# Performance work log

Hardware: AMD Instinct MI355X
Metric: run time of the kernel (lower is better)

## Reference

```python
import jax, jax.numpy as jnp
import numpy as np

D = 64          # feature dim
H_POS = 64      # pos_mlp hidden
H_ATTN = 4 * D  # attn_mlp hidden
B, N = 1, 1024


def setup_inputs() -> dict:
    key = jax.random.key(0)
    ks = jax.random.split(key, 12)
    s = lambda fan_in: 1.0 / np.sqrt(fan_in)
    return {
        "x": jax.random.normal(ks[0], (B, N, D), jnp.float32),
        "pos": jax.random.normal(ks[1], (B, N, 2), jnp.float32),
        "Wq": jax.random.normal(ks[2], (D, D), jnp.float32) * s(D),
        "Wk": jax.random.normal(ks[3], (D, D), jnp.float32) * s(D),
        "Wv": jax.random.normal(ks[4], (D, D), jnp.float32) * s(D),
        "pW1": jax.random.normal(ks[5], (2, H_POS), jnp.float32) * s(2),
        "pb1": jnp.zeros((H_POS,), jnp.float32),
        "pW2": jax.random.normal(ks[6], (H_POS, D), jnp.float32) * s(H_POS),
        "pb2": jnp.zeros((D,), jnp.float32),
        "aW1": jax.random.normal(ks[7], (D, H_ATTN), jnp.float32) * s(D),
        "ab1": jnp.zeros((H_ATTN,), jnp.float32),
        "aW2": jax.random.normal(ks[8], (H_ATTN, D), jnp.float32) * s(H_ATTN),
        "ab2": jnp.zeros((D,), jnp.float32),
    }


def reference(x, pos, Wq, Wk, Wv, pW1, pb1, pW2, pb2, aW1, ab1, aW2, ab2):
    # projections: [b, n, d]
    q = x @ Wq
    k = x @ Wk
    v = x @ Wv
    # pairwise relative positions: [b, i, j, 2]
    rel_pos = pos[:, :, None, :] - pos[:, None, :, :]
    # pos MLP: [b, i, j, d]
    rpe = jax.nn.relu(rel_pos @ pW1 + pb1) @ pW2 + pb2
    # pairwise q - k: [b, i, j, d]
    qk_rel = q[:, :, None, :] - k[:, None, :, :]
    # values broadcast over i, plus positional embedding: [b, i, j, d]
    vv = v[:, None, :, :] + rpe
    # attention MLP on (qk_rel + rpe): [b, i, j, d]
    sim = jax.nn.relu((qk_rel + rpe) @ aW1 + ab1) @ aW2 + ab2
    # softmax over j (axis=-2), per-channel
    attn = jax.nn.softmax(sim, axis=-2)
    # weighted aggregation: [b, i, d]
    agg = jnp.einsum('bijd,bijd->bid', attn, vv)
    return agg
```

## Files before the change

### kernel.cpp

```cpp
#include <hip/hip_runtime.h>


typedef float f32x4 __attribute__((ext_vector_type(4)));
using sh8 = __attribute__((ext_vector_type(8))) short;

static constexpr int NPTS = 1024;

static constexpr size_t BEXT_OFF = 0;
static constexpr size_t AW2F_OFF = 65536;
static constexpr size_t PW2F_OFF = 98304;
static constexpr size_t CARR_OFF = 106496;
static constexpr size_t AI_OFF   = 107520;
static constexpr size_t QI_OFF   = 369664;
static constexpr size_t VPT_OFF  = 631808;
static constexpr size_t AJ_OFF   = 893952;
static constexpr size_t KN_OFF   = 1025024;

__device__ __forceinline__ unsigned short f2b_rne(float f) {
    unsigned u = __float_as_uint(f);
    u += 0x7fffu + ((u >> 16) & 1u);
    return (unsigned short)(u >> 16);
}
__device__ __forceinline__ unsigned pk2(float lo, float hi) {
    return __builtin_amdgcn_perm(__float_as_uint(hi), __float_as_uint(lo), 0x07060302);
}
__device__ __forceinline__ float b2f(unsigned short s) {
    return __uint_as_float(((unsigned)s) << 16);
}

__global__ void prep_all(const float* __restrict__ x, const float* __restrict__ pos,
                         const float* __restrict__ Wq, const float* __restrict__ Wk,
                         const float* __restrict__ Wv, const float* __restrict__ pW1,
                         const float* __restrict__ pb1, const float* __restrict__ pW2,
                         const float* __restrict__ pb2, const float* __restrict__ aW1,
                         const float* __restrict__ ab1, const float* __restrict__ aW2,
                         unsigned short* __restrict__ bextf, unsigned short* __restrict__ aw2f,
                         unsigned short* __restrict__ pw2f, float* __restrict__ cArr,
                         float* __restrict__ qI, unsigned short* __restrict__ kN,
                         float* __restrict__ vPT, float* __restrict__ aI,
                         unsigned short* __restrict__ aJ)
{
    const int b = blockIdx.x;
    if (b < 209) {
        const int idx = b * 256 + threadIdx.x;
        if (idx < 32768) {
            const int k = idx >> 8, t = idx & 255;
            float val;
            if (k < 64) {
                float s = 0.f;
                for (int d = 0; d < 64; ++d) s = fmaf(pW2[k * 64 + d], aW1[d * 256 + t], s);
                val = s;
            } else {
                val = aW1[(k - 64) * 256 + t];
            }
            const int kc = k >> 5, kl = k & 31, qq = kl >> 3, e = kl & 7;
            const int ntg = t >> 4, tl = t & 15;
            bextf[(((size_t)(kc * 16 + ntg) * 64) + (qq * 16 + tl)) * 8 + e] = f2b_rne(val);
        } else if (idx < 49152) {
            const int r = idx - 32768;
            const int kp = r >> 6, d = r & 63;
            const int t = 64 * (kp >> 6) + 16 * (kp & 3) + ((kp >> 2) & 15);
            const int kc = kp >> 5, kl = kp & 31, qq = kl >> 3, e = kl & 7;
            const int nt = d >> 4, dl = d & 15;
            aw2f[(((size_t)(kc * 4 + nt) * 64) + (qq * 16 + dl)) * 8 + e] = f2b_rne(aW2[t * 64 + d]);
        } else if (idx < 53248) {
            const int r = idx - 49152;
            const int k = r >> 6, d = r & 63;
            const int kc = k >> 5, kl = k & 31, qq = kl >> 3, e = kl & 7;
            const int nt = d >> 4, dl = d & 15;
            pw2f[(((size_t)(kc * 4 + nt) * 64) + (qq * 16 + dl)) * 8 + e] = f2b_rne(pW2[k * 64 + d]);
        } else if (idx < 53504) {
            const int t = idx - 53248;
            float s = ab1[t];
            for (int d = 0; d < 64; ++d) s = fmaf(pb2[d], aW1[d * 256 + t], s);
            cArr[t] = s;
        }
    } else {
        const int t = threadIdx.x, sub = t >> 6, d = t & 63;
        const int i = (b - 209) * 4 + sub;
        __shared__ float xs[4][64];
        xs[sub][d] = x[i * 64 + d];
        __syncthreads();
        float q = 0.f, k = 0.f, v = 0.f;
        for (int e = 0; e < 64; ++e) {
            const float xe = xs[sub][e];
            q = fmaf(xe, Wq[e * 64 + d], q);
            k = fmaf(xe, Wk[e * 64 + d], k);
            v = fmaf(xe, Wv[e * 64 + d], v);
        }
        const float a = pos[i * 2] * pW1[d] + pos[i * 2 + 1] * pW1[64 + d];
        qI[i * 64 + d] = q;
        kN[i * 64 + d] = f2b_rne(-k);
        vPT[d * NPTS + i] = v + pb2[d];
        aI[i * 64 + d] = a + pb1[d];
        aJ[i * 64 + d] = f2b_rne(a);
    }
}

__global__ __launch_bounds__(256, 2) void ptl_main(
    const float* __restrict__ aI, const float* __restrict__ qI,
    const unsigned short* __restrict__ aJ, const unsigned short* __restrict__ kN,
    const float* __restrict__ vPT,
    const unsigned short* __restrict__ bextf, const unsigned short* __restrict__ aw2f,
    const unsigned short* __restrict__ pw2f, const float* __restrict__ cArr,
    float* __restrict__ out)
{
    const int i    = blockIdx.x;
    const int tid  = threadIdx.x;
    const int w    = tid >> 6;
    const int lane = tid & 63;
    const int m    = lane & 15;
    const int q    = lane >> 4;

    __shared__ __align__(16) uint4 AfL[2][2][4][64];
    __shared__ __align__(16) unsigned char Hs[2][2][16 * 528];

    sh8 Bf[16];
#pragma unroll
    for (int kc = 0; kc < 4; ++kc)
#pragma unroll
        for (int nt = 0; nt < 4; ++nt)
            Bf[kc * 4 + nt] = *(const sh8*)(bextf + ((size_t)((kc * 16 + 4 * w + nt) * 64 + lane)) * 8);
    sh8 W2f[8];
#pragma unroll
    for (int kc = 0; kc < 8; ++kc)
        W2f[kc] = *(const sh8*)(aw2f + ((size_t)((kc * 4 + w) * 64 + lane)) * 8);
    sh8 P2f[2];
#pragma unroll
    for (int kc = 0; kc < 2; ++kc)
        P2f[kc] = *(const sh8*)(pw2f + ((size_t)((kc * 4 + w) * 64 + lane)) * 8);

    f32x4 cvec[4];
#pragma unroll
    for (int nt = 0; nt < 4; ++nt) {
        const float c = cArr[64 * w + 16 * nt + m];
        cvec[nt] = (f32x4){c, c, c, c};
    }

    const int  half   = w & 1;
    const bool isRelu = (w < 2);
    const unsigned short* bsrc  = (isRelu ? aJ : kN) + m * 64 + half * 32 + q * 8;
    const float*          ibase = (isRelu ? aI : qI) + i * 64 + half * 32 + q * 8;
    float iv[8];
    *(float4*)(iv)     = *(const float4*)(ibase);
    *(float4*)(iv + 4) = *(const float4*)(ibase + 4);

#pragma unroll
    for (int s = 0; s < 2; ++s) {
        const sh8 raw = *(const sh8*)(bsrc + (size_t)(16 * s) * 64);
        float t[8];
#pragma unroll
        for (int e = 0; e < 8; ++e)
            t[e] = isRelu ? fmaxf(iv[e] - b2f((unsigned short)raw[e]), 0.f)
                          : iv[e] + b2f((unsigned short)raw[e]);
        uint4 pk;
        pk.x = pk2(t[0], t[1]); pk.y = pk2(t[2], t[3]);
        pk.z = pk2(t[4], t[5]); pk.w = pk2(t[6], t[7]);
        AfL[0][s][w][lane] = pk;
    }
    __syncthreads();

    float num = 0.f, den = 0.f;
    const f32x4 z4 = {0.f, 0.f, 0.f, 0.f};
    const float* vbase = vPT + (size_t)(16 * w + m) * NPTS;

    for (int n = 0; n < 32; ++n) {
        const int pb = n & 1, nb = pb ^ 1;
        const int j0 = n << 5;

        sh8 raw0, raw1;
        if (n < 31) {
            raw0 = *(const sh8*)(bsrc + (size_t)(j0 + 32) * 64);
            raw1 = *(const sh8*)(bsrc + (size_t)(j0 + 48) * 64);
        }
        const float4 vj0 = *(const float4*)(vbase + j0 + 4 * q);
        const float4 vj1 = *(const float4*)(vbase + j0 + 16 + 4 * q);

        const sh8 A00 = *(const sh8*)&AfL[pb][0][0][lane];
        const sh8 A01 = *(const sh8*)&AfL[pb][0][1][lane];
        const sh8 A02 = *(const sh8*)&AfL[pb][0][2][lane];
        const sh8 A03 = *(const sh8*)&AfL[pb][0][3][lane];
        {
            f32x4 acc[4];
#pragma unroll
            for (int nt = 0; nt < 4; ++nt) {
                acc[nt] = __builtin_amdgcn_mfma_f32_16x16x32_bf16(A00, Bf[0 * 4 + nt], cvec[nt], 0, 0, 0);
                acc[nt] = __builtin_amdgcn_mfma_f32_16x16x32_bf16(A01, Bf[1 * 4 + nt], acc[nt], 0, 0, 0);
                acc[nt] = __builtin_amdgcn_mfma_f32_16x16x32_bf16(A02, Bf[2 * 4 + nt], acc[nt], 0, 0, 0);
                acc[nt] = __builtin_amdgcn_mfma_f32_16x16x32_bf16(A03, Bf[3 * 4 + nt], acc[nt], 0, 0, 0);
            }
            unsigned char* hw = Hs[pb][0] + (4 * q) * 528 + 128 * w + 8 * m;
#pragma unroll
            for (int r = 0; r < 4; ++r) {
                uint2 pk;
                pk.x = pk2(fmaxf(acc[0][r], 0.f), fmaxf(acc[1][r], 0.f));
                pk.y = pk2(fmaxf(acc[2][r], 0.f), fmaxf(acc[3][r], 0.f));
                *(uint2*)(hw + r * 528) = pk;
            }
        }

        const sh8 A10 = *(const sh8*)&AfL[pb][1][0][lane];
        const sh8 A11 = *(const sh8*)&AfL[pb][1][1][lane];
        const sh8 A12 = *(const sh8*)&AfL[pb][1][2][lane];
        const sh8 A13 = *(const sh8*)&AfL[pb][1][3][lane];
        {
            f32x4 acc[4];
#pragma unroll
            for (int nt = 0; nt < 4; ++nt) {
                acc[nt] = __builtin_amdgcn_mfma_f32_16x16x32_bf16(A10, Bf[0 * 4 + nt], cvec[nt], 0, 0, 0);
                acc[nt] = __builtin_amdgcn_mfma_f32_16x16x32_bf16(A11, Bf[1 * 4 + nt], acc[nt], 0, 0, 0);
                acc[nt] = __builtin_amdgcn_mfma_f32_16x16x32_bf16(A12, Bf[2 * 4 + nt], acc[nt], 0, 0, 0);
                acc[nt] = __builtin_amdgcn_mfma_f32_16x16x32_bf16(A13, Bf[3 * 4 + nt], acc[nt], 0, 0, 0);
            }
            unsigned char* hw = Hs[pb][1] + (4 * q) * 528 + 128 * w + 8 * m;
#pragma unroll
            for (int r = 0; r < 4; ++r) {
                uint2 pk;
                pk.x = pk2(fmaxf(acc[0][r], 0.f), fmaxf(acc[1][r], 0.f));
                pk.y = pk2(fmaxf(acc[2][r], 0.f), fmaxf(acc[3][r], 0.f));
                *(uint2*)(hw + r * 528) = pk;
            }
        }

        if (n < 31) {
#pragma unroll
            for (int s = 0; s < 2; ++s) {
                const sh8 raw = s ? raw1 : raw0;
                float t[8];
#pragma unroll
                for (int e = 0; e < 8; ++e)
                    t[e] = isRelu ? fmaxf(iv[e] - b2f((unsigned short)raw[e]), 0.f)
                                  : iv[e] + b2f((unsigned short)raw[e]);
                uint4 pk;
                pk.x = pk2(t[0], t[1]); pk.y = pk2(t[2], t[3]);
                pk.z = pk2(t[4], t[5]); pk.w = pk2(t[6], t[7]);
                AfL[nb][s][w][lane] = pk;
            }
        }

        __syncthreads();

        {
            f32x4 accS = z4;
#pragma unroll
            for (int kc = 0; kc < 8; ++kc) {
                const sh8 hf = *(const sh8*)(Hs[pb][0] + m * 528 + kc * 64 + 16 * q);
                accS = __builtin_amdgcn_mfma_f32_16x16x32_bf16(hf, W2f[kc], accS, 0, 0, 0);
            }
            const f32x4 vc = {vj0.x, vj0.y, vj0.z, vj0.w};
            f32x4 accR = __builtin_amdgcn_mfma_f32_16x16x32_bf16(A00, P2f[0], vc, 0, 0, 0);
            accR = __builtin_amdgcn_mfma_f32_16x16x32_bf16(A01, P2f[1], accR, 0, 0, 0);
#pragma unroll
            for (int r = 0; r < 4; ++r) {
                const float ex = __expf(accS[r]);
                num = fmaf(ex, accR[r], num);
                den += ex;
            }
        }
        {
            f32x4 accS = z4;
#pragma unroll
            for (int kc = 0; kc < 8; ++kc) {
                const sh8 hf = *(const sh8*)(Hs[pb][1] + m * 528 + kc * 64 + 16 * q);
                accS = __builtin_amdgcn_mfma_f32_16x16x32_bf16(hf, W2f[kc], accS, 0, 0, 0);
            }
            const f32x4 vc = {vj1.x, vj1.y, vj1.z, vj1.w};
            f32x4 accR = __builtin_amdgcn_mfma_f32_16x16x32_bf16(A10, P2f[0], vc, 0, 0, 0);
            accR = __builtin_amdgcn_mfma_f32_16x16x32_bf16(A11, P2f[1], accR, 0, 0, 0);
#pragma unroll
            for (int r = 0; r < 4; ++r) {
                const float ex = __expf(accS[r]);
                num = fmaf(ex, accR[r], num);
                den += ex;
            }
        }
    }

    num += __shfl_xor(num, 16);
    num += __shfl_xor(num, 32);
    den += __shfl_xor(den, 16);
    den += __shfl_xor(den, 32);
    if (q == 0) out[i * 64 + 16 * w + m] = num / den;
}

extern "C" void kernel_launch(void* const* d_in, const int* in_sizes, int n_in,
                              void* d_out, int out_size, void* d_ws, size_t ws_size,
                              hipStream_t stream) {
    const float* x   = (const float*)d_in[0];
    const float* pos = (const float*)d_in[1];
    const float* Wq  = (const float*)d_in[2];
    const float* Wk  = (const float*)d_in[3];
    const float* Wv  = (const float*)d_in[4];
    const float* pW1 = (const float*)d_in[5];
    const float* pb1 = (const float*)d_in[6];
    const float* pW2 = (const float*)d_in[7];
    const float* pb2 = (const float*)d_in[8];
    const float* aW1 = (const float*)d_in[9];
    const float* ab1 = (const float*)d_in[10];
    const float* aW2 = (const float*)d_in[11];

    char* ws = (char*)d_ws;
    unsigned short* bextf = (unsigned short*)(ws + BEXT_OFF);
    unsigned short* aw2f  = (unsigned short*)(ws + AW2F_OFF);
    unsigned short* pw2f  = (unsigned short*)(ws + PW2F_OFF);
    float*          cArr  = (float*)(ws + CARR_OFF);
    float*          aIa   = (float*)(ws + AI_OFF);
    float*          qIa   = (float*)(ws + QI_OFF);
    float*          vPTa  = (float*)(ws + VPT_OFF);
    unsigned short* aJa   = (unsigned short*)(ws + AJ_OFF);
    unsigned short* kNa   = (unsigned short*)(ws + KN_OFF);

    prep_all<<<465, 256, 0, stream>>>(x, pos, Wq, Wk, Wv, pW1, pb1, pW2, pb2, aW1, ab1, aW2,
                                      bextf, aw2f, pw2f, cArr, qIa, kNa, vPTa, aIa, aJa);
    ptl_main<<<NPTS, 256, 0, stream>>>(aIa, qIa, aJa, kNa, vPTa, bextf, aw2f, pw2f, cArr,
                                       (float*)d_out);
}
```

Baseline: 193.0 us.

## Precompute q·aW1 and k·aW1 projections to halve first-layer MFMA K dimension

```diff
diff --git a/kernel.cpp b/kernel.cpp
--- a/kernel.cpp
+++ b/kernel.cpp
@@ -7,14 +7,13 @@
 static constexpr int NPTS = 1024;
 
 static constexpr size_t BEXT_OFF = 0;
-static constexpr size_t AW2F_OFF = 65536;
-static constexpr size_t PW2F_OFF = 98304;
-static constexpr size_t CARR_OFF = 106496;
-static constexpr size_t AI_OFF   = 107520;
-static constexpr size_t QI_OFF   = 369664;
-static constexpr size_t VPT_OFF  = 631808;
-static constexpr size_t AJ_OFF   = 893952;
-static constexpr size_t KN_OFF   = 1025024;
+static constexpr size_t AW2F_OFF = 32768;
+static constexpr size_t PW2F_OFF = 65536;
+static constexpr size_t AI_OFF   = 73728;
+static constexpr size_t AJ_OFF   = 335872;
+static constexpr size_t VPT_OFF  = 466944;
+static constexpr size_t CQ_OFF   = 729088;
+static constexpr size_t KAT_OFF  = 1777664;
 
 __device__ __forceinline__ unsigned short f2b_rne(float f) {
     unsigned u = __float_as_uint(f);
@@ -35,51 +34,41 @@
                          const float* __restrict__ pb2, const float* __restrict__ aW1,
                          const float* __restrict__ ab1, const float* __restrict__ aW2,
                          unsigned short* __restrict__ bextf, unsigned short* __restrict__ aw2f,
-                         unsigned short* __restrict__ pw2f, float* __restrict__ cArr,
-                         float* __restrict__ qI, unsigned short* __restrict__ kN,
-                         float* __restrict__ vPT, float* __restrict__ aI,
-                         unsigned short* __restrict__ aJ)
+                         unsigned short* __restrict__ pw2f,
+                         float* __restrict__ aI, unsigned short* __restrict__ aJ,
+                         float* __restrict__ vPT, float* __restrict__ cq,
+                         float* __restrict__ kaT)
 {
     const int b = blockIdx.x;
-    if (b < 209) {
+    if (b < 144) {
         const int idx = b * 256 + threadIdx.x;
-        if (idx < 32768) {
+        if (idx < 16384) {
             const int k = idx >> 8, t = idx & 255;
-            float val;
-            if (k < 64) {
-                float s = 0.f;
-                for (int d = 0; d < 64; ++d) s = fmaf(pW2[k * 64 + d], aW1[d * 256 + t], s);
-                val = s;
-            } else {
-                val = aW1[(k - 64) * 256 + t];
-            }
+            float s = 0.f;
+            for (int d = 0; d < 64; ++d) s = fmaf(pW2[k * 64 + d], aW1[d * 256 + t], s);
             const int kc = k >> 5, kl = k & 31, qq = kl >> 3, e = kl & 7;
             const int ntg = t >> 4, tl = t & 15;
-            bextf[(((size_t)(kc * 16 + ntg) * 64) + (qq * 16 + tl)) * 8 + e] = f2b_rne(val);
-        } else if (idx < 49152) {
-            const int r = idx - 32768;
+            bextf[(((size_t)(kc * 16 + ntg) * 64) + (qq * 16 + tl)) * 8 + e] = f2b_rne(s);
+        } else if (idx < 32768) {
+            const int r = idx - 16384;
             const int kp = r >> 6, d = r & 63;
             const int t = 64 * (kp >> 6) + 16 * (kp & 3) + ((kp >> 2) & 15);
             const int kc = kp >> 5, kl = kp & 31, qq = kl >> 3, e = kl & 7;
             const int nt = d >> 4, dl = d & 15;
-            aw2f[(((size_t)(kc * 4 + nt) * 64) + (qq * 16 + dl)) * 8 + e] = f2b_rne(aW2[t * 64 + d]);
-        } else if (idx < 53248) {
-            const int r = idx - 49152;
+            aw2f[(((size_t)(kc * 4 + nt) * 64) + (qq * 16 + dl)) * 8 + e] =
+                f2b_rne(aW2[t * 64 + d] * 1.4426950408889634f);
+        } else if (idx < 36864) {
+            const int r = idx - 32768;
             const int k = r >> 6, d = r & 63;
             const int kc = k >> 5, kl = k & 31, qq = kl >> 3, e = kl & 7;
             const int nt = d >> 4, dl = d & 15;
             pw2f[(((size_t)(kc * 4 + nt) * 64) + (qq * 16 + dl)) * 8 + e] = f2b_rne(pW2[k * 64 + d]);
-        } else if (idx < 53504) {
-            const int t = idx - 53248;
-            float s = ab1[t];
-            for (int d = 0; d < 64; ++d) s = fmaf(pb2[d], aW1[d * 256 + t], s);
-            cArr[t] = s;
         }
     } else {
-        const int t = threadIdx.x, sub = t >> 6, d = t & 63;
-        const int i = (b - 209) * 4 + sub;
-        __shared__ float xs[4][64];
-        xs[sub][d] = x[i * 64 + d];
+        const int tid = threadIdx.x, sub = tid >> 6, d = tid & 63;
+        const int i0 = (b - 144) * 4;
+        __shared__ float xs[4][64], qs[4][64], ks[4][64];
+        xs[sub][d] = x[(i0 + sub) * 64 + d];
         __syncthreads();
         float q = 0.f, k = 0.f, v = 0.f;
         for (int e = 0; e < 64; ++e) {
@@ -88,22 +77,45 @@
             k = fmaf(xe, Wk[e * 64 + d], k);
             v = fmaf(xe, Wv[e * 64 + d], v);
         }
-        const float a = pos[i * 2] * pW1[d] + pos[i * 2 + 1] * pW1[64 + d];
-        qI[i * 64 + d] = q;
-        kN[i * 64 + d] = f2b_rne(-k);
-        vPT[d * NPTS + i] = v + pb2[d];
-        aI[i * 64 + d] = a + pb1[d];
-        aJ[i * 64 + d] = f2b_rne(a);
+        const float a = pos[(i0 + sub) * 2] * pW1[d] + pos[(i0 + sub) * 2 + 1] * pW1[64 + d];
+        qs[sub][d] = q;
+        ks[sub][d] = k;
+        vPT[d * NPTS + i0 + sub] = v + pb2[d];
+        aI[(i0 + sub) * 64 + d] = a + pb1[d];
+        aJ[(i0 + sub) * 64 + d] = f2b_rne(a);
+        __syncthreads();
+        const int t = tid;
+        float c = ab1[t];
+        float qa0 = 0.f, qa1 = 0.f, qa2 = 0.f, qa3 = 0.f;
+        float ka0 = 0.f, ka1 = 0.f, ka2 = 0.f, ka3 = 0.f;
+        for (int dd = 0; dd < 64; ++dd) {
+            const float wv = aW1[dd * 256 + t];
+            c   = fmaf(pb2[dd],   wv, c);
+            qa0 = fmaf(qs[0][dd], wv, qa0);
+            qa1 = fmaf(qs[1][dd], wv, qa1);
+            qa2 = fmaf(qs[2][dd], wv, qa2);
+            qa3 = fmaf(qs[3][dd], wv, qa3);
+            ka0 = fmaf(ks[0][dd], wv, ka0);
+            ka1 = fmaf(ks[1][dd], wv, ka1);
+            ka2 = fmaf(ks[2][dd], wv, ka2);
+            ka3 = fmaf(ks[3][dd], wv, ka3);
+        }
+        cq[(i0 + 0) * 256 + t] = c + qa0;
+        cq[(i0 + 1) * 256 + t] = c + qa1;
+        cq[(i0 + 2) * 256 + t] = c + qa2;
+        cq[(i0 + 3) * 256 + t] = c + qa3;
+        float4 kn;
+        kn.x = -ka0; kn.y = -ka1; kn.z = -ka2; kn.w = -ka3;
+        *(float4*)(kaT + (size_t)t * NPTS + i0) = kn;
     }
 }
 
 __global__ __launch_bounds__(256, 2) void ptl_main(
-    const float* __restrict__ aI, const float* __restrict__ qI,
-    const unsigned short* __restrict__ aJ, const unsigned short* __restrict__ kN,
-    const float* __restrict__ vPT,
+    const float* __restrict__ aI, const unsigned short* __restrict__ aJ,
+    const float* __restrict__ vPT, const float* __restrict__ cq,
+    const float* __restrict__ kaT,
     const unsigned short* __restrict__ bextf, const unsigned short* __restrict__ aw2f,
-    const unsigned short* __restrict__ pw2f, const float* __restrict__ cArr,
-    float* __restrict__ out)
+    const unsigned short* __restrict__ pw2f, float* __restrict__ out)
 {
     const int i    = blockIdx.x;
     const int tid  = threadIdx.x;
@@ -111,176 +123,174 @@
     const int lane = tid & 63;
     const int m    = lane & 15;
     const int q    = lane >> 4;
-
-    __shared__ __align__(16) uint4 AfL[2][2][4][64];
+    const int js   = w >> 1;
+    const int wh   = w & 1;
+
+    __shared__ __align__(16) uint4 AfL[2][2][2][64];
     __shared__ __align__(16) unsigned char Hs[2][2][16 * 528];
-
-    sh8 Bf[16];
-#pragma unroll
-    for (int kc = 0; kc < 4; ++kc)
+    __shared__ float redN[4][2][16], redD[4][2][16];
+
+    sh8 Bf[8];
+#pragma unroll
+    for (int kc = 0; kc < 2; ++kc)
 #pragma unroll
         for (int nt = 0; nt < 4; ++nt)
             Bf[kc * 4 + nt] = *(const sh8*)(bextf + ((size_t)((kc * 16 + 4 * w + nt) * 64 + lane)) * 8);
-    sh8 W2f[8];
+    sh8 W2f[16];
 #pragma unroll
     for (int kc = 0; kc < 8; ++kc)
-        W2f[kc] = *(const sh8*)(aw2f + ((size_t)((kc * 4 + w) * 64 + lane)) * 8);
-    sh8 P2f[2];
+#pragma unroll
+        for (int nt = 0; nt < 2; ++nt)
+            W2f[kc * 2 + nt] = *(const sh8*)(aw2f + ((size_t)((kc * 4 + 2 * wh + nt) * 64 + lane)) * 8);
+    sh8 P2f[4];
 #pragma unroll
     for (int kc = 0; kc < 2; ++kc)
-        P2f[kc] = *(const sh8*)(pw2f + ((size_t)((kc * 4 + w) * 64 + lane)) * 8);
+#pragma unroll
+        for (int nt = 0; nt < 2; ++nt)
+            P2f[kc * 2 + nt] = *(const sh8*)(pw2f + ((size_t)((kc * 4 + 2 * wh + nt) * 64 + lane)) * 8);
 
     f32x4 cvec[4];
 #pragma unroll
     for (int nt = 0; nt < 4; ++nt) {
-        const float c = cArr[64 * w + 16 * nt + m];
+        const float c = cq[i * 256 + 64 * w + 16 * nt + m];
         cvec[nt] = (f32x4){c, c, c, c};
     }
 
-    const int  half   = w & 1;
-    const bool isRelu = (w < 2);
-    const unsigned short* bsrc  = (isRelu ? aJ : kN) + m * 64 + half * 32 + q * 8;
-    const float*          ibase = (isRelu ? aI : qI) + i * 64 + half * 32 + q * 8;
+    const unsigned short* bsrc  = aJ + ((size_t)(16 * js + m)) * 64 + wh * 32 + q * 8;
+    const float*          ibase = aI + i * 64 + wh * 32 + q * 8;
     float iv[8];
     *(float4*)(iv)     = *(const float4*)(ibase);
     *(float4*)(iv + 4) = *(const float4*)(ibase + 4);
 
-#pragma unroll
-    for (int s = 0; s < 2; ++s) {
-        const sh8 raw = *(const sh8*)(bsrc + (size_t)(16 * s) * 64);
+    {
+        const sh8 raw = *(const sh8*)(bsrc);
         float t[8];
 #pragma unroll
-        for (int e = 0; e < 8; ++e)
-            t[e] = isRelu ? fmaxf(iv[e] - b2f((unsigned short)raw[e]), 0.f)
-                          : iv[e] + b2f((unsigned short)raw[e]);
+        for (int e = 0; e < 8; ++e) t[e] = fmaxf(iv[e] - b2f((unsigned short)raw[e]), 0.f);
         uint4 pk;
         pk.x = pk2(t[0], t[1]); pk.y = pk2(t[2], t[3]);
         pk.z = pk2(t[4], t[5]); pk.w = pk2(t[6], t[7]);
-        AfL[0][s][w][lane] = pk;
+        AfL[0][js][wh][lane] = pk;
     }
     __syncthreads();
 
-    float num = 0.f, den = 0.f;
+    float num0 = 0.f, num1 = 0.f, den0 = 0.f, den1 = 0.f;
     const f32x4 z4 = {0.f, 0.f, 0.f, 0.f};
-    const float* vbase = vPT + (size_t)(16 * w + m) * NPTS;
+    const float* vb0 = vPT + (size_t)(32 * wh + m) * NPTS + 16 * js + 4 * q;
+    const float* vb1 = vPT + (size_t)(32 * wh + 16 + m) * NPTS + 16 * js + 4 * q;
+    const float* kbase = kaT + (size_t)(64 * w + m) * NPTS + 4 * q;
 
     for (int n = 0; n < 32; ++n) {
         const int pb = n & 1, nb = pb ^ 1;
         const int j0 = n << 5;
 
-        sh8 raw0, raw1;
-        if (n < 31) {
-            raw0 = *(const sh8*)(bsrc + (size_t)(j0 + 32) * 64);
-            raw1 = *(const sh8*)(bsrc + (size_t)(j0 + 48) * 64);
-        }
-        const float4 vj0 = *(const float4*)(vbase + j0 + 4 * q);
-        const float4 vj1 = *(const float4*)(vbase + j0 + 16 + 4 * q);
+        sh8 raw;
+        if (n < 31) raw = *(const sh8*)(bsrc + (size_t)(j0 + 32) * 64);
+        f32x4 ka0[4];
+#pragma unroll
+        for (int nt = 0; nt < 4; ++nt)
+            ka0[nt] = *(const f32x4*)(kbase + (size_t)(16 * nt) * NPTS + j0);
+        const float4 vj0 = *(const float4*)(vb0 + j0);
+        const float4 vj1 = *(const float4*)(vb1 + j0);
 
         const sh8 A00 = *(const sh8*)&AfL[pb][0][0][lane];
         const sh8 A01 = *(const sh8*)&AfL[pb][0][1][lane];
-        const sh8 A02 = *(const sh8*)&AfL[pb][0][2][lane];
-        const sh8 A03 = *(const sh8*)&AfL[pb][0][3][lane];
+        const sh8 A10 = *(const sh8*)&AfL[pb][1][0][lane];
+        const sh8 A11 = *(const sh8*)&AfL[pb][1][1][lane];
+
         {
             f32x4 acc[4];
 #pragma unroll
             for (int nt = 0; nt < 4; ++nt) {
-                acc[nt] = __builtin_amdgcn_mfma_f32_16x16x32_bf16(A00, Bf[0 * 4 + nt], cvec[nt], 0, 0, 0);
-                acc[nt] = __builtin_amdgcn_mfma_f32_16x16x32_bf16(A01, Bf[1 * 4 + nt], acc[nt], 0, 0, 0);
-                acc[nt] = __builtin_amdgcn_mfma_f32_16x16x32_bf16(A02, Bf[2 * 4 + nt], acc[nt], 0, 0, 0);
-                acc[nt] = __builtin_amdgcn_mfma_f32_16x16x32_bf16(A03, Bf[3 * 4 + nt], acc[nt], 0, 0, 0);
+                acc[nt] = __builtin_amdgcn_mfma_f32_16x16x32_bf16(A00, Bf[nt], cvec[nt], 0, 0, 0);
+                acc[nt] = __builtin_amdgcn_mfma_f32_16x16x32_bf16(A01, Bf[4 + nt], acc[nt], 0, 0, 0);
             }
             unsigned char* hw = Hs[pb][0] + (4 * q) * 528 + 128 * w + 8 * m;
 #pragma unroll
             for (int r = 0; r < 4; ++r) {
                 uint2 pk;
-                pk.x = pk2(fmaxf(acc[0][r], 0.f), fmaxf(acc[1][r], 0.f));
-                pk.y = pk2(fmaxf(acc[2][r], 0.f), fmaxf(acc[3][r], 0.f));
+                pk.x = pk2(fmaxf(acc[0][r] + ka0[0][r], 0.f), fmaxf(acc[1][r] + ka0[1][r], 0.f));
+                pk.y = pk2(fmaxf(acc[2][r] + ka0[2][r], 0.f), fmaxf(acc[3][r] + ka0[3][r], 0.f));
                 *(uint2*)(hw + r * 528) = pk;
             }
         }
-
-        const sh8 A10 = *(const sh8*)&AfL[pb][1][0][lane];
-        const sh8 A11 = *(const sh8*)&AfL[pb][1][1][lane];
-        const sh8 A12 = *(const sh8*)&AfL[pb][1][2][lane];
-        const sh8 A13 = *(const sh8*)&AfL[pb][1][3][lane];
+        f32x4 ka1[4];
+#pragma unroll
+        for (int nt = 0; nt < 4; ++nt)
+            ka1[nt] = *(const f32x4*)(kbase + (size_t)(16 * nt) * NPTS + j0 + 16);
+
         {
             f32x4 acc[4];
 #pragma unroll
             for (int nt = 0; nt < 4; ++nt) {
-                acc[nt] = __builtin_amdgcn_mfma_f32_16x16x32_bf16(A10, Bf[0 * 4 + nt], cvec[nt], 0, 0, 0);
-                acc[nt] = __builtin_amdgcn_mfma_f32_16x16x32_bf16(A11, Bf[1 * 4 + nt], acc[nt], 0, 0, 0);
-                acc[nt] = __builtin_amdgcn_mfma_f32_16x16x32_bf16(A12, Bf[2 * 4 + nt], acc[nt], 0, 0, 0);
-                acc[nt] = __builtin_amdgcn_mfma_f32_16x16x32_bf16(A13, Bf[3 * 4 + nt], acc[nt], 0, 0, 0);
+                acc[nt] = __builtin_amdgcn_mfma_f32_16x16x32_bf16(A10, Bf[nt], cvec[nt], 0, 0, 0);
+                acc[nt] = __builtin_amdgcn_mfma_f32_16x16x32_bf16(A11, Bf[4 + nt], acc[nt], 0, 0, 0);
             }
             unsigned char* hw = Hs[pb][1] + (4 * q) * 528 + 128 * w + 8 * m;
 #pragma unroll
             for (int r = 0; r < 4; ++r) {
                 uint2 pk;
-                pk.x = pk2(fmaxf(acc[0][r], 0.f), fmaxf(acc[1][r], 0.f));
-                pk.y = pk2(fmaxf(acc[2][r], 0.f), fmaxf(acc[3][r], 0.f));
+                pk.x = pk2(fmaxf(acc[0][r] + ka1[0][r], 0.f), fmaxf(acc[1][r] + ka1[1][r], 0.f));
+                pk.y = pk2(fmaxf(acc[2][r] + ka1[2][r], 0.f), fmaxf(acc[3][r] + ka1[3][r], 0.f));
                 *(uint2*)(hw + r * 528) = pk;
             }
         }
 
         if (n < 31) {
-#pragma unroll
-            for (int s = 0; s < 2; ++s) {
-                const sh8 raw = s ? raw1 : raw0;
-                float t[8];
-#pragma unroll
-                for (int e = 0; e < 8; ++e)
-                    t[e] = isRelu ? fmaxf(iv[e] - b2f((unsigned short)raw[e]), 0.f)
-                                  : iv[e] + b2f((unsigned short)raw[e]);
-                uint4 pk;
-                pk.x = pk2(t[0], t[1]); pk.y = pk2(t[2], t[3]);
-                pk.z = pk2(t[4], t[5]); pk.w = pk2(t[6], t[7]);
-                AfL[nb][s][w][lane] = pk;
-            }
+            float t[8];
+#pragma unroll
+            for (int e = 0; e < 8; ++e) t[e] = fmaxf(iv[e] - b2f((unsigned short)raw[e]), 0.f);
+            uint4 pk;
+            pk.x = pk2(t[0], t[1]); pk.y = pk2(t[2], t[3]);
+            pk.z = pk2(t[4], t[5]); pk.w = pk2(t[6], t[7]);
+            AfL[nb][js][wh][lane] = pk;
         }
 
         __syncthreads();
 
-        {
-            f32x4 accS = z4;
-#pragma unroll
-            for (int kc = 0; kc < 8; ++kc) {
-                const sh8 hf = *(const sh8*)(Hs[pb][0] + m * 528 + kc * 64 + 16 * q);
-                accS = __builtin_amdgcn_mfma_f32_16x16x32_bf16(hf, W2f[kc], accS, 0, 0, 0);
-            }
-            const f32x4 vc = {vj0.x, vj0.y, vj0.z, vj0.w};
-            f32x4 accR = __builtin_amdgcn_mfma_f32_16x16x32_bf16(A00, P2f[0], vc, 0, 0, 0);
-            accR = __builtin_amdgcn_mfma_f32_16x16x32_bf16(A01, P2f[1], accR, 0, 0, 0);
-#pragma unroll
-            for (int r = 0; r < 4; ++r) {
-                const float ex = __expf(accS[r]);
-                num = fmaf(ex, accR[r], num);
-                den += ex;
-            }
-        }
-        {
-            f32x4 accS = z4;
-#pragma unroll
-            for (int kc = 0; kc < 8; ++kc) {
-                const sh8 hf = *(const sh8*)(Hs[pb][1] + m * 528 + kc * 64 + 16 * q);
-                accS = __builtin_amdgcn_mfma_f32_16x16x32_bf16(hf, W2f[kc], accS, 0, 0, 0);
-            }
-            const f32x4 vc = {vj1.x, vj1.y, vj1.z, vj1.w};
-            f32x4 accR = __builtin_amdgcn_mfma_f32_16x16x32_bf16(A10, P2f[0], vc, 0, 0, 0);
-            accR = __builtin_amdgcn_mfma_f32_16x16x32_bf16(A11, P2f[1], accR, 0, 0, 0);
-#pragma unroll
-            for (int r = 0; r < 4; ++r) {
-                const float ex = __expf(accS[r]);
-                num = fmaf(ex, accR[r], num);
-                den += ex;
-            }
-        }
-    }
-
-    num += __shfl_xor(num, 16);
-    num += __shfl_xor(num, 32);
-    den += __shfl_xor(den, 16);
-    den += __shfl_xor(den, 32);
-    if (q == 0) out[i * 64 + 16 * w + m] = num / den;
+        f32x4 aS0 = z4, aS1 = z4;
+        const unsigned char* hb = Hs[pb][js] + m * 528 + 16 * q;
+#pragma unroll
+        for (int kc = 0; kc < 8; ++kc) {
+            const sh8 hf = *(const sh8*)(hb + kc * 64);
+            aS0 = __builtin_amdgcn_mfma_f32_16x16x32_bf16(hf, W2f[kc * 2 + 0], aS0, 0, 0, 0);
+            aS1 = __builtin_amdgcn_mfma_f32_16x16x32_bf16(hf, W2f[kc * 2 + 1], aS1, 0, 0, 0);
+        }
+        const sh8 G3a = js ? A10 : A00;
+        const sh8 G3b = js ? A11 : A01;
+        const f32x4 vc0 = {vj0.x, vj0.y, vj0.z, vj0.w};
+        const f32x4 vc1 = {vj1.x, vj1.y, vj1.z, vj1.w};
+        f32x4 aR0 = __builtin_amdgcn_mfma_f32_16x16x32_bf16(G3a, P2f[0], vc0, 0, 0, 0);
+        aR0 = __builtin_amdgcn_mfma_f32_16x16x32_bf16(G3b, P2f[2], aR0, 0, 0, 0);
+        f32x4 aR1 = __builtin_amdgcn_mfma_f32_16x16x32_bf16(G3a, P2f[1], vc1, 0, 0, 0);
+        aR1 = __builtin_amdgcn_mfma_f32_16x16x32_bf16(G3b, P2f[3], aR1, 0, 0, 0);
+
+#pragma unroll
+        for (int r = 0; r < 4; ++r) {
+            const float e0 = exp2f(aS0[r]);
+            num0 = fmaf(e0, aR0[r], num0);
+            den0 += e0;
+            const float e1 = exp2f(aS1[r]);
+            num1 = fmaf(e1, aR1[r], num1);
+            den1 += e1;
+        }
+    }
+
+    num0 += __shfl_xor(num0, 16); num0 += __shfl_xor(num0, 32);
+    num1 += __shfl_xor(num1, 16); num1 += __shfl_xor(num1, 32);
+    den0 += __shfl_xor(den0, 16); den0 += __shfl_xor(den0, 32);
+    den1 += __shfl_xor(den1, 16); den1 += __shfl_xor(den1, 32);
+    if (q == 0) {
+        redN[w][0][m] = num0; redN[w][1][m] = num1;
+        redD[w][0][m] = den0; redD[w][1][m] = den1;
+    }
+    __syncthreads();
+    if (tid < 64) {
+        const int d = tid, h = d >> 5, ntf = (d >> 4) & 1, mf = d & 15;
+        const float nn = redN[h][ntf][mf] + redN[2 + h][ntf][mf];
+        const float dd = redD[h][ntf][mf] + redD[2 + h][ntf][mf];
+        out[i * 64 + d] = nn / dd;
+    }
 }
 
 extern "C" void kernel_launch(void* const* d_in, const int* in_sizes, int n_in,
@@ -303,15 +313,14 @@
     unsigned short* bextf = (unsigned short*)(ws + BEXT_OFF);
     unsigned short* aw2f  = (unsigned short*)(ws + AW2F_OFF);
     unsigned short* pw2f  = (unsigned short*)(ws + PW2F_OFF);
-    float*          cArr  = (float*)(ws + CARR_OFF);
     float*          aIa   = (float*)(ws + AI_OFF);
-    float*          qIa   = (float*)(ws + QI_OFF);
+    unsigned short* aJa   = (unsigned short*)(ws + AJ_OFF);
     float*          vPTa  = (float*)(ws + VPT_OFF);
-    unsigned short* aJa   = (unsigned short*)(ws + AJ_OFF);
-    unsigned short* kNa   = (unsigned short*)(ws + KN_OFF);
-
-    prep_all<<<465, 256, 0, stream>>>(x, pos, Wq, Wk, Wv, pW1, pb1, pW2, pb2, aW1, ab1, aW2,
-                                      bextf, aw2f, pw2f, cArr, qIa, kNa, vPTa, aIa, aJa);
-    ptl_main<<<NPTS, 256, 0, stream>>>(aIa, qIa, aJa, kNa, vPTa, bextf, aw2f, pw2f, cArr,
+    float*          cqa   = (float*)(ws + CQ_OFF);
+    float*          kaTa  = (float*)(ws + KAT_OFF);
+
+    prep_all<<<400, 256, 0, stream>>>(x, pos, Wq, Wk, Wv, pW1, pb1, pW2, pb2, aW1, ab1, aW2,
+                                      bextf, aw2f, pw2f, aIa, aJa, vPTa, cqa, kaTa);
+    ptl_main<<<NPTS, 256, 0, stream>>>(aIa, aJa, vPTa, cqa, kaTa, bextf, aw2f, pw2f,
                                        (float*)d_out);
 }
```

Result: slower. 254.9 us (+32.1%).

## Split second-layer GEMM by j-half and channel pair per wave, fold log2e into aW2

Applied to the files above, without the earlier changes.

```diff
diff --git a/kernel.cpp b/kernel.cpp
--- a/kernel.cpp
+++ b/kernel.cpp
@@ -62,7 +62,8 @@
             const int t = 64 * (kp >> 6) + 16 * (kp & 3) + ((kp >> 2) & 15);
             const int kc = kp >> 5, kl = kp & 31, qq = kl >> 3, e = kl & 7;
             const int nt = d >> 4, dl = d & 15;
-            aw2f[(((size_t)(kc * 4 + nt) * 64) + (qq * 16 + dl)) * 8 + e] = f2b_rne(aW2[t * 64 + d]);
+            aw2f[(((size_t)(kc * 4 + nt) * 64) + (qq * 16 + dl)) * 8 + e] =
+                f2b_rne(aW2[t * 64 + d] * 1.4426950408889634f);
         } else if (idx < 53248) {
             const int r = idx - 49152;
             const int k = r >> 6, d = r & 63;
@@ -111,9 +112,12 @@
     const int lane = tid & 63;
     const int m    = lane & 15;
     const int q    = lane >> 4;
+    const int js   = w >> 1;
+    const int wh   = w & 1;
 
     __shared__ __align__(16) uint4 AfL[2][2][4][64];
     __shared__ __align__(16) unsigned char Hs[2][2][16 * 528];
+    __shared__ float redN[4][2][16], redD[4][2][16];
 
     sh8 Bf[16];
 #pragma unroll
@@ -121,21 +125,22 @@
 #pragma unroll
         for (int nt = 0; nt < 4; ++nt)
             Bf[kc * 4 + nt] = *(const sh8*)(bextf + ((size_t)((kc * 16 + 4 * w + nt) * 64 + lane)) * 8);
-    sh8 W2f[8];
+    sh8 W2f[16];
 #pragma unroll
     for (int kc = 0; kc < 8; ++kc)
-        W2f[kc] = *(const sh8*)(aw2f + ((size_t)((kc * 4 + w) * 64 + lane)) * 8);
-    sh8 P2f[2];
+#pragma unroll
+        for (int nt = 0; nt < 2; ++nt)
+            W2f[kc * 2 + nt] = *(const sh8*)(aw2f + ((size_t)((kc * 4 + 2 * wh + nt) * 64 + lane)) * 8);
+    sh8 P2f[4];
 #pragma unroll
     for (int kc = 0; kc < 2; ++kc)
-        P2f[kc] = *(const sh8*)(pw2f + ((size_t)((kc * 4 + w) * 64 + lane)) * 8);
-
-    f32x4 cvec[4];
-#pragma unroll
-    for (int nt = 0; nt < 4; ++nt) {
-        const float c = cArr[64 * w + 16 * nt + m];
-        cvec[nt] = (f32x4){c, c, c, c};
-    }
+#pragma unroll
+        for (int nt = 0; nt < 2; ++nt)
+            P2f[kc * 2 + nt] = *(const sh8*)(pw2f + ((size_t)((kc * 4 + 2 * wh + nt) * 64 + lane)) * 8);
+
+    float creg[4];
+#pragma unroll
+    for (int nt = 0; nt < 4; ++nt) creg[nt] = cArr[64 * w + 16 * nt + m];
 
     const int  half   = w & 1;
     const bool isRelu = (w < 2);
@@ -160,9 +165,10 @@
     }
     __syncthreads();
 
-    float num = 0.f, den = 0.f;
+    float num0 = 0.f, num1 = 0.f, den0 = 0.f, den1 = 0.f;
     const f32x4 z4 = {0.f, 0.f, 0.f, 0.f};
-    const float* vbase = vPT + (size_t)(16 * w + m) * NPTS;
+    const float* vb0 = vPT + (size_t)(32 * wh + m) * NPTS + 16 * js + 4 * q;
+    const float* vb1 = vPT + (size_t)(32 * wh + 16 + m) * NPTS + 16 * js + 4 * q;
 
     for (int n = 0; n < 32; ++n) {
         const int pb = n & 1, nb = pb ^ 1;
@@ -173,8 +179,8 @@
             raw0 = *(const sh8*)(bsrc + (size_t)(j0 + 32) * 64);
             raw1 = *(const sh8*)(bsrc + (size_t)(j0 + 48) * 64);
         }
-        const float4 vj0 = *(const float4*)(vbase + j0 + 4 * q);
-        const float4 vj1 = *(const float4*)(vbase + j0 + 16 + 4 * q);
+        const float4 vj0 = *(const float4*)(vb0 + j0);
+        const float4 vj1 = *(const float4*)(vb1 + j0);
 
         const sh8 A00 = *(const sh8*)&AfL[pb][0][0][lane];
         const sh8 A01 = *(const sh8*)&AfL[pb][0][1][lane];
@@ -184,7 +190,8 @@
             f32x4 acc[4];
 #pragma unroll
             for (int nt = 0; nt < 4; ++nt) {
-                acc[nt] = __builtin_amdgcn_mfma_f32_16x16x32_bf16(A00, Bf[0 * 4 + nt], cvec[nt], 0, 0, 0);
+                const f32x4 cv = {creg[nt], creg[nt], creg[nt], creg[nt]};
+                acc[nt] = __builtin_amdgcn_mfma_f32_16x16x32_bf16(A00, Bf[0 * 4 + nt], cv, 0, 0, 0);
                 acc[nt] = __builtin_amdgcn_mfma_f32_16x16x32_bf16(A01, Bf[1 * 4 + nt], acc[nt], 0, 0, 0);
                 acc[nt] = __builtin_amdgcn_mfma_f32_16x16x32_bf16(A02, Bf[2 * 4 + nt], acc[nt], 0, 0, 0);
                 acc[nt] = __builtin_amdgcn_mfma_f32_16x16x32_bf16(A03, Bf[3 * 4 + nt], acc[nt], 0, 0, 0);
@@ -207,7 +214,8 @@
             f32x4 acc[4];
 #pragma unroll
             for (int nt = 0; nt < 4; ++nt) {
-                acc[nt] = __builtin_amdgcn_mfma_f32_16x16x32_bf16(A10, Bf[0 * 4 + nt], cvec[nt], 0, 0, 0);
+                const f32x4 cv = {creg[nt], creg[nt], creg[nt], creg[nt]};
+                acc[nt] = __builtin_amdgcn_mfma_f32_16x16x32_bf16(A10, Bf[0 * 4 + nt], cv, 0, 0, 0);
                 acc[nt] = __builtin_amdgcn_mfma_f32_16x16x32_bf16(A11, Bf[1 * 4 + nt], acc[nt], 0, 0, 0);
                 acc[nt] = __builtin_amdgcn_mfma_f32_16x16x32_bf16(A12, Bf[2 * 4 + nt], acc[nt], 0, 0, 0);
                 acc[nt] = __builtin_amdgcn_mfma_f32_16x16x32_bf16(A13, Bf[3 * 4 + nt], acc[nt], 0, 0, 0);
@@ -240,47 +248,49 @@
 
         __syncthreads();
 
-        {
-            f32x4 accS = z4;
-#pragma unroll
-            for (int kc = 0; kc < 8; ++kc) {
-                const sh8 hf = *(const sh8*)(Hs[pb][0] + m * 528 + kc * 64 + 16 * q);
-                accS = __builtin_amdgcn_mfma_f32_16x16x32_bf16(hf, W2f[kc], accS, 0, 0, 0);
-            }
-            const f32x4 vc = {vj0.x, vj0.y, vj0.z, vj0.w};
-            f32x4 accR = __builtin_amdgcn_mfma_f32_16x16x32_bf16(A00, P2f[0], vc, 0, 0, 0);
-            accR = __builtin_amdgcn_mfma_f32_16x16x32_bf16(A01, P2f[1], accR, 0, 0, 0);
-#pragma unroll
-            for (int r = 0; r < 4; ++r) {
-                const float ex = __expf(accS[r]);
-                num = fmaf(ex, accR[r], num);
-                den += ex;
-            }
-        }
-        {
-            f32x4 accS = z4;
-#pragma unroll
-            for (int kc = 0; kc < 8; ++kc) {
-                const sh8 hf = *(const sh8*)(Hs[pb][1] + m * 528 + kc * 64 + 16 * q);
-                accS = __builtin_amdgcn_mfma_f32_16x16x32_bf16(hf, W2f[kc], accS, 0, 0, 0);
-            }
-            const f32x4 vc = {vj1.x, vj1.y, vj1.z, vj1.w};
-            f32x4 accR = __builtin_amdgcn_mfma_f32_16x16x32_bf16(A10, P2f[0], vc, 0, 0, 0);
-            accR = __builtin_amdgcn_mfma_f32_16x16x32_bf16(A11, P2f[1], accR, 0, 0, 0);
-#pragma unroll
-            for (int r = 0; r < 4; ++r) {
-                const float ex = __expf(accS[r]);
-                num = fmaf(ex, accR[r], num);
-                den += ex;
-            }
-        }
-    }
-
-    num += __shfl_xor(num, 16);
-    num += __shfl_xor(num, 32);
-    den += __shfl_xor(den, 16);
-    den += __shfl_xor(den, 32);
-    if (q == 0) out[i * 64 + 16 * w + m] = num / den;
+        f32x4 aS0 = z4, aS1 = z4;
+        const unsigned char* hb = Hs[pb][js] + m * 528 + 16 * q;
+#pragma unroll
+        for (int kc = 0; kc < 8; ++kc) {
+            const sh8 hf = *(const sh8*)(hb + kc * 64);
+            aS0 = __builtin_amdgcn_mfma_f32_16x16x32_bf16(hf, W2f[kc * 2 + 0], aS0, 0, 0, 0);
+            aS1 = __builtin_amdgcn_mfma_f32_16x16x32_bf16(hf, W2f[kc * 2 + 1], aS1, 0, 0, 0);
+        }
+        const sh8 G3a = js ? A10 : A00;
+        const sh8 G3b = js ? A11 : A01;
+        const f32x4 vc0 = {vj0.x, vj0.y, vj0.z, vj0.w};
+        const f32x4 vc1 = {vj1.x, vj1.y, vj1.z, vj1.w};
+        f32x4 aR0 = __builtin_amdgcn_mfma_f32_16x16x32_bf16(G3a, P2f[0], vc0, 0, 0, 0);
+        aR0 = __builtin_amdgcn_mfma_f32_16x16x32_bf16(G3b, P2f[2], aR0, 0, 0, 0);
+        f32x4 aR1 = __builtin_amdgcn_mfma_f32_16x16x32_bf16(G3a, P2f[1], vc1, 0, 0, 0);
+        aR1 = __builtin_amdgcn_mfma_f32_16x16x32_bf16(G3b, P2f[3], aR1, 0, 0, 0);
+
+#pragma unroll
+        for (int r = 0; r < 4; ++r) {
+            const float e0 = exp2f(aS0[r]);
+            num0 = fmaf(e0, aR0[r], num0);
+            den0 += e0;
+            const float e1 = exp2f(aS1[r]);
+            num1 = fmaf(e1, aR1[r], num1);
+            den1 += e1;
+        }
+    }
+
+    num0 += __shfl_xor(num0, 16); num0 += __shfl_xor(num0, 32);
+    num1 += __shfl_xor(num1, 16); num1 += __shfl_xor(num1, 32);
+    den0 += __shfl_xor(den0, 16); den0 += __shfl_xor(den0, 32);
+    den1 += __shfl_xor(den1, 16); den1 += __shfl_xor(den1, 32);
+    if (q == 0) {
+        redN[w][0][m] = num0; redN[w][1][m] = num1;
+        redD[w][0][m] = den0; redD[w][1][m] = den1;
+    }
+    __syncthreads();
+    if (tid < 64) {
+        const int d = tid, h = d >> 5, ntf = (d >> 4) & 1, mf = d & 15;
+        const float nn = redN[h][ntf][mf] + redN[2 + h][ntf][mf];
+        const float dd = redD[h][ntf][mf] + redD[2 + h][ntf][mf];
+        out[i * 64 + d] = nn / dd;
+    }
 }
 
 extern "C" void kernel_launch(void* const* d_in, const int* in_sizes, int n_in,
```

New measurement: 201.3 us. 1.04x slower.

## Software-pipeline attention MLP stages across iterations and fold log2e into aW2

Applied to the files above, without the earlier changes.

```diff
diff --git a/kernel.cpp b/kernel.cpp
--- a/kernel.cpp
+++ b/kernel.cpp
@@ -62,7 +62,8 @@
             const int t = 64 * (kp >> 6) + 16 * (kp & 3) + ((kp >> 2) & 15);
             const int kc = kp >> 5, kl = kp & 31, qq = kl >> 3, e = kl & 7;
             const int nt = d >> 4, dl = d & 15;
-            aw2f[(((size_t)(kc * 4 + nt) * 64) + (qq * 16 + dl)) * 8 + e] = f2b_rne(aW2[t * 64 + d]);
+            aw2f[(((size_t)(kc * 4 + nt) * 64) + (qq * 16 + dl)) * 8 + e] =
+                f2b_rne(aW2[t * 64 + d] * 1.4426950408889634f);
         } else if (idx < 53248) {
             const int r = idx - 49152;
             const int k = r >> 6, d = r & 63;
@@ -130,12 +131,9 @@
     for (int kc = 0; kc < 2; ++kc)
         P2f[kc] = *(const sh8*)(pw2f + ((size_t)((kc * 4 + w) * 64 + lane)) * 8);
 
-    f32x4 cvec[4];
-#pragma unroll
-    for (int nt = 0; nt < 4; ++nt) {
-        const float c = cArr[64 * w + 16 * nt + m];
-        cvec[nt] = (f32x4){c, c, c, c};
-    }
+    float creg[4];
+#pragma unroll
+    for (int nt = 0; nt < 4; ++nt) creg[nt] = cArr[64 * w + 16 * nt + m];
 
     const int  half   = w & 1;
     const bool isRelu = (w < 2);
@@ -164,32 +162,30 @@
     const f32x4 z4 = {0.f, 0.f, 0.f, 0.f};
     const float* vbase = vPT + (size_t)(16 * w + m) * NPTS;
 
-    for (int n = 0; n < 32; ++n) {
-        const int pb = n & 1, nb = pb ^ 1;
-        const int j0 = n << 5;
-
-        sh8 raw0, raw1;
-        if (n < 31) {
-            raw0 = *(const sh8*)(bsrc + (size_t)(j0 + 32) * 64);
-            raw1 = *(const sh8*)(bsrc + (size_t)(j0 + 48) * 64);
-        }
-        const float4 vj0 = *(const float4*)(vbase + j0 + 4 * q);
-        const float4 vj1 = *(const float4*)(vbase + j0 + 16 + 4 * q);
-
-        const sh8 A00 = *(const sh8*)&AfL[pb][0][0][lane];
-        const sh8 A01 = *(const sh8*)&AfL[pb][0][1][lane];
-        const sh8 A02 = *(const sh8*)&AfL[pb][0][2][lane];
-        const sh8 A03 = *(const sh8*)&AfL[pb][0][3][lane];
+    sh8 pA00, pA01, pA10, pA11;
+    float vjp[8];
+
+    {
+        const sh8 A00 = *(const sh8*)&AfL[0][0][0][lane];
+        const sh8 A01 = *(const sh8*)&AfL[0][0][1][lane];
+        const sh8 A02 = *(const sh8*)&AfL[0][0][2][lane];
+        const sh8 A03 = *(const sh8*)&AfL[0][0][3][lane];
+        const sh8 A10 = *(const sh8*)&AfL[0][1][0][lane];
+        const sh8 A11 = *(const sh8*)&AfL[0][1][1][lane];
+        const sh8 A12 = *(const sh8*)&AfL[0][1][2][lane];
+        const sh8 A13 = *(const sh8*)&AfL[0][1][3][lane];
+        pA00 = A00; pA01 = A01; pA10 = A10; pA11 = A11;
         {
             f32x4 acc[4];
 #pragma unroll
             for (int nt = 0; nt < 4; ++nt) {
-                acc[nt] = __builtin_amdgcn_mfma_f32_16x16x32_bf16(A00, Bf[0 * 4 + nt], cvec[nt], 0, 0, 0);
+                const f32x4 cv = {creg[nt], creg[nt], creg[nt], creg[nt]};
+                acc[nt] = __builtin_amdgcn_mfma_f32_16x16x32_bf16(A00, Bf[0 * 4 + nt], cv, 0, 0, 0);
                 acc[nt] = __builtin_amdgcn_mfma_f32_16x16x32_bf16(A01, Bf[1 * 4 + nt], acc[nt], 0, 0, 0);
                 acc[nt] = __builtin_amdgcn_mfma_f32_16x16x32_bf16(A02, Bf[2 * 4 + nt], acc[nt], 0, 0, 0);
                 acc[nt] = __builtin_amdgcn_mfma_f32_16x16x32_bf16(A03, Bf[3 * 4 + nt], acc[nt], 0, 0, 0);
             }
-            unsigned char* hw = Hs[pb][0] + (4 * q) * 528 + 128 * w + 8 * m;
+            unsigned char* hw = Hs[0][0] + (4 * q) * 528 + 128 * w + 8 * m;
 #pragma unroll
             for (int r = 0; r < 4; ++r) {
                 uint2 pk;
@@ -198,16 +194,95 @@
                 *(uint2*)(hw + r * 528) = pk;
             }
         }
-
+        {
+            f32x4 acc[4];
+#pragma unroll
+            for (int nt = 0; nt < 4; ++nt) {
+                const f32x4 cv = {creg[nt], creg[nt], creg[nt], creg[nt]};
+                acc[nt] = __builtin_amdgcn_mfma_f32_16x16x32_bf16(A10, Bf[0 * 4 + nt], cv, 0, 0, 0);
+                acc[nt] = __builtin_amdgcn_mfma_f32_16x16x32_bf16(A11, Bf[1 * 4 + nt], acc[nt], 0, 0, 0);
+                acc[nt] = __builtin_amdgcn_mfma_f32_16x16x32_bf16(A12, Bf[2 * 4 + nt], acc[nt], 0, 0, 0);
+                acc[nt] = __builtin_amdgcn_mfma_f32_16x16x32_bf16(A13, Bf[3 * 4 + nt], acc[nt], 0, 0, 0);
+            }
+            unsigned char* hw = Hs[0][1] + (4 * q) * 528 + 128 * w + 8 * m;
+#pragma unroll
+            for (int r = 0; r < 4; ++r) {
+                uint2 pk;
+                pk.x = pk2(fmaxf(acc[0][r], 0.f), fmaxf(acc[1][r], 0.f));
+                pk.y = pk2(fmaxf(acc[2][r], 0.f), fmaxf(acc[3][r], 0.f));
+                *(uint2*)(hw + r * 528) = pk;
+            }
+        }
+#pragma unroll
+        for (int s = 0; s < 2; ++s) {
+            const sh8 raw = *(const sh8*)(bsrc + (size_t)(32 + 16 * s) * 64);
+            float t[8];
+#pragma unroll
+            for (int e = 0; e < 8; ++e)
+                t[e] = isRelu ? fmaxf(iv[e] - b2f((unsigned short)raw[e]), 0.f)
+                              : iv[e] + b2f((unsigned short)raw[e]);
+            uint4 pk;
+            pk.x = pk2(t[0], t[1]); pk.y = pk2(t[2], t[3]);
+            pk.z = pk2(t[4], t[5]); pk.w = pk2(t[6], t[7]);
+            AfL[1][s][w][lane] = pk;
+        }
+        *(float4*)(vjp)     = *(const float4*)(vbase + 4 * q);
+        *(float4*)(vjp + 4) = *(const float4*)(vbase + 16 + 4 * q);
+    }
+    __syncthreads();
+
+    for (int n = 1; n < 32; ++n) {
+        const int pb = n & 1, hb = pb ^ 1;
+        const int j0 = n << 5;
+
+        sh8 Hf[8];
+#pragma unroll
+        for (int kc = 0; kc < 8; ++kc)
+            Hf[kc] = *(const sh8*)(Hs[hb][0] + m * 528 + kc * 64 + 16 * q);
+
+        const sh8 A00 = *(const sh8*)&AfL[pb][0][0][lane];
+        const sh8 A01 = *(const sh8*)&AfL[pb][0][1][lane];
+        const sh8 A02 = *(const sh8*)&AfL[pb][0][2][lane];
+        const sh8 A03 = *(const sh8*)&AfL[pb][0][3][lane];
         const sh8 A10 = *(const sh8*)&AfL[pb][1][0][lane];
         const sh8 A11 = *(const sh8*)&AfL[pb][1][1][lane];
         const sh8 A12 = *(const sh8*)&AfL[pb][1][2][lane];
         const sh8 A13 = *(const sh8*)&AfL[pb][1][3][lane];
+
+        sh8 raw0, raw1;
+        if (n < 31) {
+            raw0 = *(const sh8*)(bsrc + (size_t)(j0 + 32) * 64);
+            raw1 = *(const sh8*)(bsrc + (size_t)(j0 + 48) * 64);
+        }
+        float vjc[8];
+        *(float4*)(vjc)     = *(const float4*)(vbase + j0 + 4 * q);
+        *(float4*)(vjc + 4) = *(const float4*)(vbase + j0 + 16 + 4 * q);
+
         {
             f32x4 acc[4];
 #pragma unroll
             for (int nt = 0; nt < 4; ++nt) {
-                acc[nt] = __builtin_amdgcn_mfma_f32_16x16x32_bf16(A10, Bf[0 * 4 + nt], cvec[nt], 0, 0, 0);
+                const f32x4 cv = {creg[nt], creg[nt], creg[nt], creg[nt]};
+                acc[nt] = __builtin_amdgcn_mfma_f32_16x16x32_bf16(A00, Bf[0 * 4 + nt], cv, 0, 0, 0);
+                acc[nt] = __builtin_amdgcn_mfma_f32_16x16x32_bf16(A01, Bf[1 * 4 + nt], acc[nt], 0, 0, 0);
+                acc[nt] = __builtin_amdgcn_mfma_f32_16x16x32_bf16(A02, Bf[2 * 4 + nt], acc[nt], 0, 0, 0);
+                acc[nt] = __builtin_amdgcn_mfma_f32_16x16x32_bf16(A03, Bf[3 * 4 + nt], acc[nt], 0, 0, 0);
+            }
+            unsigned char* hw = Hs[pb][0] + (4 * q) * 528 + 128 * w + 8 * m;
+#pragma unroll
+            for (int r = 0; r < 4; ++r) {
+                uint2 pk;
+                pk.x = pk2(fmaxf(acc[0][r], 0.f), fmaxf(acc[1][r], 0.f));
+                pk.y = pk2(fmaxf(acc[2][r], 0.f), fmaxf(acc[3][r], 0.f));
+                *(uint2*)(hw + r * 528) = pk;
+            }
+        }
+        {
+            f32x4 acc[4];
+#pragma unroll
+            for (int nt = 0; nt < 4; ++nt) {
+                const f32x4 cv = {creg[nt], creg[nt], creg[nt], creg[nt]};
+                acc[nt] = __builtin_amdgcn_mfma_f32_16x16x32_bf16(A10, Bf[0 * 4 + nt], cv, 0, 0, 0);
                 acc[nt] = __builtin_amdgcn_mfma_f32_16x16x32_bf16(A11, Bf[1 * 4 + nt], acc[nt], 0, 0, 0);
                 acc[nt] = __builtin_amdgcn_mfma_f32_16x16x32_bf16(A12, Bf[2 * 4 + nt], acc[nt], 0, 0, 0);
                 acc[nt] = __builtin_amdgcn_mfma_f32_16x16x32_bf16(A13, Bf[3 * 4 + nt], acc[nt], 0, 0, 0);
@@ -234,45 +309,67 @@
                 uint4 pk;
                 pk.x = pk2(t[0], t[1]); pk.y = pk2(t[2], t[3]);
                 pk.z = pk2(t[4], t[5]); pk.w = pk2(t[6], t[7]);
-                AfL[nb][s][w][lane] = pk;
-            }
-        }
+                AfL[hb][s][w][lane] = pk;
+            }
+        }
+
+        f32x4 aS0 = z4;
+#pragma unroll
+        for (int kc = 0; kc < 8; ++kc)
+            aS0 = __builtin_amdgcn_mfma_f32_16x16x32_bf16(Hf[kc], W2f[kc], aS0, 0, 0, 0);
+        f32x4 aS1 = z4;
+#pragma unroll
+        for (int kc = 0; kc < 8; ++kc) {
+            const sh8 hf = *(const sh8*)(Hs[hb][1] + m * 528 + kc * 64 + 16 * q);
+            aS1 = __builtin_amdgcn_mfma_f32_16x16x32_bf16(hf, W2f[kc], aS1, 0, 0, 0);
+        }
+        const f32x4 vc0 = {vjp[0], vjp[1], vjp[2], vjp[3]};
+        const f32x4 vc1 = {vjp[4], vjp[5], vjp[6], vjp[7]};
+        f32x4 aR0 = __builtin_amdgcn_mfma_f32_16x16x32_bf16(pA00, P2f[0], vc0, 0, 0, 0);
+        aR0 = __builtin_amdgcn_mfma_f32_16x16x32_bf16(pA01, P2f[1], aR0, 0, 0, 0);
+        f32x4 aR1 = __builtin_amdgcn_mfma_f32_16x16x32_bf16(pA10, P2f[0], vc1, 0, 0, 0);
+        aR1 = __builtin_amdgcn_mfma_f32_16x16x32_bf16(pA11, P2f[1], aR1, 0, 0, 0);
+
+#pragma unroll
+        for (int r = 0; r < 4; ++r) {
+            const float e0 = exp2f(aS0[r]);
+            num = fmaf(e0, aR0[r], num);
+            den += e0;
+            const float e1 = exp2f(aS1[r]);
+            num = fmaf(e1, aR1[r], num);
+            den += e1;
+        }
+
+        pA00 = A00; pA01 = A01; pA10 = A10; pA11 = A11;
+#pragma unroll
+        for (int e = 0; e < 8; ++e) vjp[e] = vjc[e];
 
         __syncthreads();
-
-        {
-            f32x4 accS = z4;
-#pragma unroll
-            for (int kc = 0; kc < 8; ++kc) {
-                const sh8 hf = *(const sh8*)(Hs[pb][0] + m * 528 + kc * 64 + 16 * q);
-                accS = __builtin_amdgcn_mfma_f32_16x16x32_bf16(hf, W2f[kc], accS, 0, 0, 0);
-            }
-            const f32x4 vc = {vj0.x, vj0.y, vj0.z, vj0.w};
-            f32x4 accR = __builtin_amdgcn_mfma_f32_16x16x32_bf16(A00, P2f[0], vc, 0, 0, 0);
-            accR = __builtin_amdgcn_mfma_f32_16x16x32_bf16(A01, P2f[1], accR, 0, 0, 0);
-#pragma unroll
-            for (int r = 0; r < 4; ++r) {
-                const float ex = __expf(accS[r]);
-                num = fmaf(ex, accR[r], num);
-                den += ex;
-            }
-        }
-        {
-            f32x4 accS = z4;
-#pragma unroll
-            for (int kc = 0; kc < 8; ++kc) {
-                const sh8 hf = *(const sh8*)(Hs[pb][1] + m * 528 + kc * 64 + 16 * q);
-                accS = __builtin_amdgcn_mfma_f32_16x16x32_bf16(hf, W2f[kc], accS, 0, 0, 0);
-            }
-            const f32x4 vc = {vj1.x, vj1.y, vj1.z, vj1.w};
-            f32x4 accR = __builtin_amdgcn_mfma_f32_16x16x32_bf16(A10, P2f[0], vc, 0, 0, 0);
-            accR = __builtin_amdgcn_mfma_f32_16x16x32_bf16(A11, P2f[1], accR, 0, 0, 0);
-#pragma unroll
-            for (int r = 0; r < 4; ++r) {
-                const float ex = __expf(accS[r]);
-                num = fmaf(ex, accR[r], num);
-                den += ex;
-            }
+    }
+
+    {
+        f32x4 aS0 = z4, aS1 = z4;
+#pragma unroll
+        for (int kc = 0; kc < 8; ++kc) {
+            const sh8 hf0 = *(const sh8*)(Hs[1][0] + m * 528 + kc * 64 + 16 * q);
+            aS0 = __builtin_amdgcn_mfma_f32_16x16x32_bf16(hf0, W2f[kc], aS0, 0, 0, 0);
+            const sh8 hf1 = *(const sh8*)(Hs[1][1] + m * 528 + kc * 64 + 16 * q);
+            aS1 = __builtin_amdgcn_mfma_f32_16x16x32_bf16(hf1, W2f[kc], aS1, 0, 0, 0);
+        }
+        const f32x4 vc0 = {vjp[0], vjp[1], vjp[2], vjp[3]};
+        const f32x4 vc1 = {vjp[4], vjp[5], vjp[6], vjp[7]};
+        f32x4 aR0 = __builtin_amdgcn_mfma_f32_16x16x32_bf16(pA00, P2f[0], vc0, 0, 0, 0);
+        aR0 = __builtin_amdgcn_mfma_f32_16x16x32_bf16(pA01, P2f[1], aR0, 0, 0, 0);
+        f32x4 aR1 = __builtin_amdgcn_mfma_f32_16x16x32_bf16(pA10, P2f[0], vc1, 0, 0, 0);
+        aR1 = __builtin_amdgcn_mfma_f32_16x16x32_bf16(pA11, P2f[1], aR1, 0, 0, 0);
+#pragma unroll
+        for (int r = 0; r < 4; ++r) {
+            const float e0 = exp2f(aS0[r]);
+            num = fmaf(e0, aR0[r], num);
+            den += e0;
+            const float e1 = exp2f(aS1[r]);
+            num = fmaf(e1, aR1[r], num);
+            den += e1;
         }
     }
 
```

Measured after the change: 201.3 us. +4.3%, slower.
